# Optimization experiments

Hardware: AMD Instinct MI355X
Metric: run time of the kernel (lower is better)

The kernel has to match this reference:

```python
import jax, jax.numpy as jnp
import numpy as np

B, F, K, E = 8, 128, 256, 256  # batch, n_features, time_step (K nodes), embed_dim=2*F
ALPHA = 0.2  # LeakyReLU negative slope


def setup_inputs() -> dict:
    key = jax.random.key(0)
    k1, k2, k3, k4, k5 = jax.random.split(key, 5)
    x = jax.random.normal(k1, (B, F, K), dtype=jnp.float32)
    W = jax.random.normal(k2, (2 * F, E), dtype=jnp.float32) * 0.05   # lin_transform.weight^T
    b_lin = jax.random.normal(k3, (E,), dtype=jnp.float32) * 0.05     # lin_transform.bias
    a = jax.random.normal(k4, (E, 1), dtype=jnp.float32) * 0.1        # attention vector
    bias = jax.random.normal(k5, (K, K), dtype=jnp.float32) * 0.05    # score bias
    return {"x": x, "W": W, "b_lin": b_lin, "a": a, "bias": bias}


def reference(x, W, b_lin, a, bias):
    # x: [B, F, K] -> v: [B, K, F]
    v = jnp.transpose(x, (0, 2, 1))
    # Linear over concat(v_i, v_j) decomposes into two per-node projections:
    # lin([v_i; v_j]) = v_i @ W[:F] + v_j @ W[F:] + b_lin  (same math, no KxKx2F concat)
    p = v @ W[:F]   # [B, K, E] (repeat_interleave half)
    q = v @ W[F:]   # [B, K, E] (repeat half)
    h = jax.nn.leaky_relu(p[:, :, None, :] + q[:, None, :, :] + b_lin, negative_slope=ALPHA)  # [B,K,K,E]
    e = jnp.squeeze(h @ a, axis=3) + bias  # [B, K, K]
    attn = jax.nn.softmax(e, axis=2)       # dropout p=0 -> identity
    h_time = jax.nn.sigmoid(attn @ v)      # [B, K, F]
    return jnp.transpose(h_time, (0, 2, 1))  # [B, F, K]
```

## Files before the change

kernel.cpp:

```cpp
#include <hip/hip_runtime.h>
#include <math.h>

#define BB 8
#define FF 128
#define KK 256
#define EE 256
#define TI 4

typedef float f4 __attribute__((ext_vector_type(4)));
typedef float f2 __attribute__((ext_vector_type(2)));

__device__ __forceinline__ float rdl(float v, int l) {
  return __int_as_float(__builtin_amdgcn_readlane(__float_as_int(v), l));
}
__device__ __forceinline__ f2 splat2(float x) { return (f2){x, x}; }
__device__ __forceinline__ f2 pkabs(f2 s) { return __builtin_elementwise_max(s, -s); }

__global__ __launch_bounds__(512, 2) void prep_kernel(
    const float* __restrict__ x, const float* __restrict__ W,
    const float* __restrict__ b_lin, const float* __restrict__ a,
    float* __restrict__ p, float* __restrict__ qT,
    float* __restrict__ xT, float* __restrict__ Q6) {
  __shared__ float xs[FF][8];
  __shared__ float part[16][EE];

  const int b  = blockIdx.x & 7;
  const int k0 = (blockIdx.x >> 3) * 8;
  const int t  = threadIdx.x;

  {
    const float* xb = x + b * FF * KK + k0;
    const int f = t >> 3, u = t & 7;
    xs[f][u]      = xb[f * KK + u];
    xs[f + 64][u] = xb[(f + 64) * KK + u];
  }
  __syncthreads();

  {
    const int u = t >> 6, f2i = (t & 63) * 2;
    f2 v; v.x = xs[f2i][u]; v.y = xs[f2i + 1][u];
    *(f2*)&xT[(b * KK + k0 + u) * FF + f2i] = v;
  }

  const int e = t & 255, fh = t >> 8;
  f2 pacc[4] = {{0,0},{0,0},{0,0},{0,0}}, qacc[4] = {{0,0},{0,0},{0,0},{0,0}};
  {
    const float* Wp = W + (fh * 64) * EE + e;
    const float* Wq = W + (FF + fh * 64) * EE + e;
    const float* xr = &xs[fh * 64][0];
#pragma unroll 8
    for (int ff = 0; ff < 64; ++ff) {
      const float w1 = Wp[ff * EE];
      const float w2 = Wq[ff * EE];
      const f4 xv0 = *(const f4*)(xr + ff * 8);
      const f4 xv1 = *(const f4*)(xr + ff * 8 + 4);
      const f2 xp0 = (f2){xv0[0], xv0[1]}, xp1 = (f2){xv0[2], xv0[3]};
      const f2 xp2 = (f2){xv1[0], xv1[1]}, xp3 = (f2){xv1[2], xv1[3]};
      const f2 w1s = splat2(w1), w2s = splat2(w2);
      pacc[0] = xp0 * w1s + pacc[0];
      pacc[1] = xp1 * w1s + pacc[1];
      pacc[2] = xp2 * w1s + pacc[2];
      pacc[3] = xp3 * w1s + pacc[3];
      qacc[0] = xp0 * w2s + qacc[0];
      qacc[1] = xp1 * w2s + qacc[1];
      qacc[2] = xp2 * w2s + qacc[2];
      qacc[3] = xp3 * w2s + qacc[3];
    }
  }

  if (fh == 1) {
#pragma unroll
    for (int u2 = 0; u2 < 4; ++u2) {
      part[2 * u2][e]     = pacc[u2].x;  part[2 * u2 + 1][e] = pacc[u2].y;
      part[8 + 2 * u2][e] = qacc[u2].x;  part[9 + 2 * u2][e] = qacc[u2].y;
    }
  }
  __syncthreads();
  if (fh == 0) {
    const float bl = b_lin[e], ae = a[e];
#pragma unroll
    for (int u2 = 0; u2 < 4; ++u2) {
#pragma unroll
      for (int h = 0; h < 2; ++h) {
        const int u = 2 * u2 + h;
        const float pv = (h ? pacc[u2].y : pacc[u2].x) + part[u][e] + bl;
        const float qv = (h ? qacc[u2].y : qacc[u2].x) + part[8 + u][e];
        p[(b * KK + k0 + u) * EE + e] = pv;
        part[u][e]     = ae * qv;
        part[8 + u][e] = qv;
      }
    }
  }
  __syncthreads();

  {
    const int ee = t >> 1, k4 = (t & 1) * 4;
    f4 v;
#pragma unroll
    for (int u = 0; u < 4; ++u) v[u] = part[8 + k4 + u][ee];
    *(f4*)&qT[(b * EE + ee) * KK + k0 + k4] = v;
  }

  {
    const int w = t >> 6, lane = t & 63;
    float s = part[w][lane] + part[w][lane + 64] + part[w][lane + 128] + part[w][lane + 192];
#pragma unroll
    for (int off = 32; off; off >>= 1) s += __shfl_xor(s, off, 64);
    if (lane == 0) Q6[b * KK + k0 + w] = 0.6f * s;
  }
}

__global__ __launch_bounds__(512, 4) void attn_kernel(
    const float* __restrict__ p, const float* __restrict__ qT,
    const float* __restrict__ xT, const float* __restrict__ Q6,
    const float* __restrict__ a, const float* __restrict__ bias,
    float* __restrict__ out) {
  __shared__ float pt[TI][EE];
  __shared__ float a_s[EE];
  __shared__ float red[4][TI][KK];
  __shared__ float sc[TI][KK];
  __shared__ float pvp[8][TI][132];

  const int b    = blockIdx.x & 7;
  const int i0   = (blockIdx.x >> 3) * TI;
  const int t    = threadIdx.x;
  const int w    = t >> 6;
  const int lane = t & 63;

  if (t < 256) {
    const int i = t >> 6, e4 = (t & 63) * 4;
    *(f4*)&pt[i][e4] = *(const f4*)&p[(b * KK + i0 + i) * EE + e4];
  } else if (t < 320) {
    const int e4 = (t - 256) * 4;
    *(f4*)&a_s[e4] = *(const f4*)&a[e4];
  }

  const int eq = w >> 1, jh = w & 1;
  const int e0 = eq * 64;
  const float* qc = qT + (b * EE + e0) * KK + jh * 128 + 2 * lane;
  f2 q0 = *(const f2*)(qc);
  f2 q1 = *(const f2*)(qc + KK);
  f2 q2 = *(const f2*)(qc + 2 * KK);
  f2 q3 = *(const f2*)(qc + 3 * KK);
  qc += 4 * KK;
  __syncthreads();

  f4 av = *(const f4*)&a_s[e0];
  f4 pv[TI];
#pragma unroll
  for (int i = 0; i < TI; ++i) pv[i] = *(const f4*)&pt[i][e0];

  {
    f2 acc[TI] = {{0,0},{0,0},{0,0},{0,0}};
#pragma unroll 4
    for (int c = 0; c < 16; ++c) {
      const f2 n0 = *(const f2*)(qc);
      const f2 n1 = *(const f2*)(qc + KK);
      const f2 n2 = *(const f2*)(qc + 2 * KK);
      const f2 n3 = *(const f2*)(qc + 3 * KK);
      qc += 4 * KK;
      const int cn = e0 + ((c + 1) & 15) * 4;
      const f4 avn = *(const f4*)&a_s[cn];
      f4 pvn[TI];
#pragma unroll
      for (int i = 0; i < TI; ++i) pvn[i] = *(const f4*)&pt[i][cn];
#pragma unroll
      for (int i = 0; i < TI; ++i) {
        const f2 s0 = pkabs(q0 + pv[i][0]);
        const f2 s1 = pkabs(q1 + pv[i][1]);
        const f2 s2 = pkabs(q2 + pv[i][2]);
        const f2 s3 = pkabs(q3 + pv[i][3]);
        acc[i] = s0 * splat2(av[0]) + acc[i];
        acc[i] = s1 * splat2(av[1]) + acc[i];
        acc[i] = s2 * splat2(av[2]) + acc[i];
        acc[i] = s3 * splat2(av[3]) + acc[i];
      }
      q0 = n0; q1 = n1; q2 = n2; q3 = n3;
      av = avn;
#pragma unroll
      for (int i = 0; i < TI; ++i) pv[i] = pvn[i];
    }
    const int jb = jh * 128 + 2 * lane;
#pragma unroll
    for (int i = 0; i < TI; ++i)
      *(f2*)&red[eq][i][jb] = acc[i];
  }
  __syncthreads();

  const int j0 = 32 * w;
  const float* xb = xT + (b * KK + j0) * FF + 2 * lane;
  f2 xv = *(const f2*)(xb);

  if (w < TI) {
    const int i = w;
    f4 s = (f4){0.f, 0.f, 0.f, 0.f};
#pragma unroll
    for (int e8 = 0; e8 < 4; ++e8)
      s += *(const f4*)&red[e8][i][4 * lane];
    const f4 q6 = *(const f4*)&Q6[b * KK + 4 * lane];
    const f4 bv = *(const f4*)&bias[(i0 + i) * KK + 4 * lane];
    f4 ev;
#pragma unroll
    for (int v = 0; v < 4; ++v)
      ev[v] = __expf(0.4f * s[v] + q6[v] + bv[v]);
    float tot = ev[0] + ev[1] + ev[2] + ev[3];
#pragma unroll
    for (int off = 32; off; off >>= 1) tot += __shfl_xor(tot, off, 64);
    const float inv = 1.f / tot;
#pragma unroll
    for (int v = 0; v < 4; ++v) ev[v] *= inv;
    *(f4*)&sc[i][4 * lane] = ev;
  }
  __syncthreads();

  {
    float rv[TI];
#pragma unroll
    for (int i = 0; i < TI; ++i) rv[i] = sc[i][j0 + (lane & 31)];
    f2 pacc[TI] = {{0,0},{0,0},{0,0},{0,0}};
#pragma unroll 4
    for (int jj = 0; jj < 32; ++jj) {
      const f2 nx = *(const f2*)(xb + (jj + 1) * FF);
#pragma unroll
      for (int i = 0; i < TI; ++i) {
        const float sv = rdl(rv[i], jj);
        pacc[i] = splat2(sv) * xv + pacc[i];
      }
      xv = nx;
    }
#pragma unroll
    for (int i = 0; i < TI; ++i)
      *(f2*)&pvp[w][i][2 * lane] = pacc[i];
  }
  __syncthreads();

  {
    const int f = t >> 2, i = t & 3;
    float s = 0.f;
#pragma unroll
    for (int jo = 0; jo < 8; ++jo) s += pvp[jo][i][f];
    out[(b * FF + f) * KK + i0 + i] = 1.f / (1.f + __expf(-s));
  }
}

extern "C" void kernel_launch(void* const* d_in, const int* in_sizes, int n_in,
                              void* d_out, int out_size, void* d_ws, size_t ws_size,
                              hipStream_t stream) {
  const float* x     = (const float*)d_in[0];
  const float* W     = (const float*)d_in[1];
  const float* b_lin = (const float*)d_in[2];
  const float* a     = (const float*)d_in[3];
  const float* bias  = (const float*)d_in[4];
  float* out = (float*)d_out;

  float* p  = (float*)d_ws;
  float* qT = p  + BB * KK * EE;
  float* xT = qT + BB * EE * KK;
  float* Q6 = xT + BB * KK * FF;

  prep_kernel<<<(KK / 8) * 8, 512, 0, stream>>>(x, W, b_lin, a, p, qT, xT, Q6);
  attn_kernel<<<(KK / TI) * 8, 512, 0, stream>>>(p, qT, xT, Q6, a, bias, out);
}
```

Measured before the change: 27.25 us.

## Halve attention row tile, raise occupancy, use scalar FMAs and early bias loads

Reduces the per-block query-row tile from 4 to 2, doubling the grid and raising the launch-bounds occupancy hint. The score loop drops the software-prefetched register copies of p and a, reads them from LDS each iteration, and replaces packed f2 abs/FMA with scalar fabsf/fmaf. Q6 and bias loads are hoisted before the first barrier to overlap their latency, and the output write becomes one f2 store per feature. The trade-off is that each streamed qT and xT element is reused across half as many rows, so total global and L2 traffic for those arrays roughly doubles, and packed-math throughput is given up.

```diff
diff --git a/kernel.cpp b/kernel.cpp
--- a/kernel.cpp
+++ b/kernel.cpp
@@ -5,7 +5,7 @@
 #define FF 128
 #define KK 256
 #define EE 256
-#define TI 4
+#define TI 2
 
 typedef float f4 __attribute__((ext_vector_type(4)));
 typedef float f2 __attribute__((ext_vector_type(2)));
@@ -14,7 +14,6 @@
   return __int_as_float(__builtin_amdgcn_readlane(__float_as_int(v), l));
 }
 __device__ __forceinline__ f2 splat2(float x) { return (f2){x, x}; }
-__device__ __forceinline__ f2 pkabs(f2 s) { return __builtin_elementwise_max(s, -s); }
 
 __global__ __launch_bounds__(512, 2) void prep_kernel(
     const float* __restrict__ x, const float* __restrict__ W,
@@ -110,7 +109,7 @@
   }
 }
 
-__global__ __launch_bounds__(512, 4) void attn_kernel(
+__global__ __launch_bounds__(512, 8) void attn_kernel(
     const float* __restrict__ p, const float* __restrict__ qT,
     const float* __restrict__ xT, const float* __restrict__ Q6,
     const float* __restrict__ a, const float* __restrict__ bias,
@@ -127,12 +126,18 @@
   const int w    = t >> 6;
   const int lane = t & 63;
 
-  if (t < 256) {
+  if (t < 128) {
     const int i = t >> 6, e4 = (t & 63) * 4;
     *(f4*)&pt[i][e4] = *(const f4*)&p[(b * KK + i0 + i) * EE + e4];
-  } else if (t < 320) {
-    const int e4 = (t - 256) * 4;
+  } else if (t < 192) {
+    const int e4 = (t - 128) * 4;
     *(f4*)&a_s[e4] = *(const f4*)&a[e4];
+  }
+
+  f4 q6v = (f4){0.f, 0.f, 0.f, 0.f}, bv = (f4){0.f, 0.f, 0.f, 0.f};
+  if (w < TI) {
+    q6v = *(const f4*)&Q6[b * KK + 4 * lane];
+    bv  = *(const f4*)&bias[(i0 + w) * KK + 4 * lane];
   }
 
   const int eq = w >> 1, jh = w & 1;
@@ -145,40 +150,29 @@
   qc += 4 * KK;
   __syncthreads();
 
-  f4 av = *(const f4*)&a_s[e0];
-  f4 pv[TI];
-#pragma unroll
-  for (int i = 0; i < TI; ++i) pv[i] = *(const f4*)&pt[i][e0];
-
-  {
-    f2 acc[TI] = {{0,0},{0,0},{0,0},{0,0}};
-#pragma unroll 4
+  {
+    f2 acc[TI] = {{0,0},{0,0}};
+#pragma unroll 2
     for (int c = 0; c < 16; ++c) {
       const f2 n0 = *(const f2*)(qc);
       const f2 n1 = *(const f2*)(qc + KK);
       const f2 n2 = *(const f2*)(qc + 2 * KK);
       const f2 n3 = *(const f2*)(qc + 3 * KK);
       qc += 4 * KK;
-      const int cn = e0 + ((c + 1) & 15) * 4;
-      const f4 avn = *(const f4*)&a_s[cn];
-      f4 pvn[TI];
-#pragma unroll
-      for (int i = 0; i < TI; ++i) pvn[i] = *(const f4*)&pt[i][cn];
+      const f4 av = *(const f4*)&a_s[e0 + 4 * c];
 #pragma unroll
       for (int i = 0; i < TI; ++i) {
-        const f2 s0 = pkabs(q0 + pv[i][0]);
-        const f2 s1 = pkabs(q1 + pv[i][1]);
-        const f2 s2 = pkabs(q2 + pv[i][2]);
-        const f2 s3 = pkabs(q3 + pv[i][3]);
-        acc[i] = s0 * splat2(av[0]) + acc[i];
-        acc[i] = s1 * splat2(av[1]) + acc[i];
-        acc[i] = s2 * splat2(av[2]) + acc[i];
-        acc[i] = s3 * splat2(av[3]) + acc[i];
+        const f4 pv = *(const f4*)&pt[i][e0 + 4 * c];
+        acc[i].x = fmaf(fabsf(q0.x + pv[0]), av[0], acc[i].x);
+        acc[i].y = fmaf(fabsf(q0.y + pv[0]), av[0], acc[i].y);
+        acc[i].x = fmaf(fabsf(q1.x + pv[1]), av[1], acc[i].x);
+        acc[i].y = fmaf(fabsf(q1.y + pv[1]), av[1], acc[i].y);
+        acc[i].x = fmaf(fabsf(q2.x + pv[2]), av[2], acc[i].x);
+        acc[i].y = fmaf(fabsf(q2.y + pv[2]), av[2], acc[i].y);
+        acc[i].x = fmaf(fabsf(q3.x + pv[3]), av[3], acc[i].x);
+        acc[i].y = fmaf(fabsf(q3.y + pv[3]), av[3], acc[i].y);
       }
       q0 = n0; q1 = n1; q2 = n2; q3 = n3;
-      av = avn;
-#pragma unroll
-      for (int i = 0; i < TI; ++i) pv[i] = pvn[i];
     }
     const int jb = jh * 128 + 2 * lane;
 #pragma unroll
@@ -197,12 +191,10 @@
 #pragma unroll
     for (int e8 = 0; e8 < 4; ++e8)
       s += *(const f4*)&red[e8][i][4 * lane];
-    const f4 q6 = *(const f4*)&Q6[b * KK + 4 * lane];
-    const f4 bv = *(const f4*)&bias[(i0 + i) * KK + 4 * lane];
     f4 ev;
 #pragma unroll
     for (int v = 0; v < 4; ++v)
-      ev[v] = __expf(0.4f * s[v] + q6[v] + bv[v]);
+      ev[v] = __expf(0.4f * s[v] + q6v[v] + bv[v]);
     float tot = ev[0] + ev[1] + ev[2] + ev[3];
 #pragma unroll
     for (int off = 32; off; off >>= 1) tot += __shfl_xor(tot, off, 64);
@@ -217,14 +209,15 @@
     float rv[TI];
 #pragma unroll
     for (int i = 0; i < TI; ++i) rv[i] = sc[i][j0 + (lane & 31)];
-    f2 pacc[TI] = {{0,0},{0,0},{0,0},{0,0}};
+    f2 pacc[TI] = {{0,0},{0,0}};
 #pragma unroll 4
     for (int jj = 0; jj < 32; ++jj) {
       const f2 nx = *(const f2*)(xb + (jj + 1) * FF);
 #pragma unroll
       for (int i = 0; i < TI; ++i) {
         const float sv = rdl(rv[i], jj);
-        pacc[i] = splat2(sv) * xv + pacc[i];
+        pacc[i].x = fmaf(sv, xv.x, pacc[i].x);
+        pacc[i].y = fmaf(sv, xv.y, pacc[i].y);
       }
       xv = nx;
     }
@@ -234,12 +227,18 @@
   }
   __syncthreads();
 
-  {
-    const int f = t >> 2, i = t & 3;
-    float s = 0.f;
-#pragma unroll
-    for (int jo = 0; jo < 8; ++jo) s += pvp[jo][i][f];
-    out[(b * FF + f) * KK + i0 + i] = 1.f / (1.f + __expf(-s));
+  if (t < FF) {
+    const int f = t;
+    f2 s = {0.f, 0.f};
+#pragma unroll
+    for (int jo = 0; jo < 8; ++jo) {
+      s.x += pvp[jo][0][f];
+      s.y += pvp[jo][1][f];
+    }
+    f2 o;
+    o.x = 1.f / (1.f + __expf(-s.x));
+    o.y = 1.f / (1.f + __expf(-s.y));
+    *(f2*)&out[(b * FF + f) * KK + i0] = o;
   }
 }
 
```

Measured after the change: 37.48 us. 37.5% more time.
